# Kernel tuning notes

Measured on AMD Instinct MI355X. Metric: run time of the kernel, lower is better.

## Reference

```python
import jax, jax.numpy as jnp
import numpy as np

N_NODES = 100000
N_EDGES = 1600000
D = 32


def setup_inputs() -> dict:
    key = jax.random.key(0)
    k1, k2, k3, k4, k5, k6, k7 = jax.random.split(key, 7)
    x = jax.random.normal(k1, (N_NODES, D), dtype=jnp.float32)
    edge_index = jax.random.randint(k2, (2, N_EDGES), 0, N_NODES, dtype=jnp.int64)
    edge_weight = jax.random.uniform(k3, (N_EDGES,), dtype=jnp.float32)
    s = 1.0 / np.sqrt(D)
    W1 = jax.random.uniform(k4, (D, D), jnp.float32, -s, s)
    b1 = jax.random.uniform(k5, (D,), jnp.float32, -s, s)
    W2 = jax.random.uniform(k6, (D, D), jnp.float32, -s, s)
    b2 = jax.random.uniform(k7, (D,), jnp.float32, -s, s)
    return {"x": x, "edge_index": edge_index, "edge_weight": edge_weight,
            "W1": W1, "b1": b1, "W2": W2, "b2": b2}


def reference(x, edge_index, edge_weight, W1, b1, W2, b2):
    N = x.shape[0]
    src, dst = edge_index[0], edge_index[1]
    # gcn_norm with improved=True: self-loops get fill value 2.0
    loops = jnp.arange(N, dtype=edge_index.dtype)
    src_a = jnp.concatenate([src, loops])
    dst_a = jnp.concatenate([dst, loops])
    w_a = jnp.concatenate([edge_weight, jnp.full((N,), 2.0, x.dtype)])
    deg = jax.ops.segment_sum(w_a, dst_a, num_segments=N)          # [N]
    dinv = jnp.where(deg > 0, jax.lax.rsqrt(deg), 0.0)             # deg^-1/2, inf->0
    norm = dinv[src_a] * w_a * dinv[dst_a]                          # [E+N]

    def gcn_conv(h, W, b):
        h = h @ W                                                   # [N,D] dense transform
        msg = h[src_a] * norm[:, None]                              # gather + normalize [E+N,D]
        return jax.ops.segment_sum(msg, dst_a, num_segments=N) + b  # scatter-add + bias

    h = jax.nn.relu(gcn_conv(x, W1, b1))
    h = jax.nn.relu(gcn_conv(h, W2, b2))
    # F.dropout treated as identity (deterministic inference reference)
    return h
```

## Files before the change

kernel.cpp:

```cpp
#include <hip/hip_runtime.h>

#define D       32
#define BS      256
#define CBLK    500
#define CBLKP   500
#define BSH     7
#define BNODES  128
#define MAXBUCK 1024
#define SBUF_CAP 3584
#define ECAP    2560
#define POISON_BASE ((int)0xAAAAAAAAu)

__device__ inline unsigned bf16pack2(float a, float b) {
    unsigned ua = __float_as_uint(a);
    unsigned ub = __float_as_uint(b);
    ua = (ua + 0x7FFFu + ((ua >> 16) & 1)) >> 16;
    ub = (ub + 0x7FFFu + ((ub >> 16) & 1)) >> 16;
    return ua | (ub << 16);
}
__device__ inline uint2 bf16pack4(float4 v) {
    return make_uint2(bf16pack2(v.x, v.y), bf16pack2(v.z, v.w));
}
__device__ inline float4 bf16unpack4(uint2 h) {
    return make_float4(__uint_as_float(h.x << 16),
                       __uint_as_float(h.x & 0xFFFF0000u),
                       __uint_as_float(h.y << 16),
                       __uint_as_float(h.y & 0xFFFF0000u));
}

__device__ inline int lds_excl_scan(int* arr, int L, int* wsum, int t) {
    int carryv = 0;
    for (int base = 0; base < L; base += BS) {
        int idx = base + t;
        int v = (idx < L) ? arr[idx] : 0;
        int incl = v;
#pragma unroll
        for (int off = 1; off < 64; off <<= 1) {
            int u = __shfl_up(incl, off, 64);
            if ((t & 63) >= off) incl += u;
        }
        if ((t & 63) == 63) wsum[t >> 6] = incl;
        __syncthreads();
        int myw = t >> 6;
        int wpre = 0;
        if (myw > 0) wpre += wsum[0];
        if (myw > 1) wpre += wsum[1];
        if (myw > 2) wpre += wsum[2];
        int tot = wsum[0] + wsum[1] + wsum[2] + wsum[3];
        if (idx < L) arr[idx] = carryv + wpre + incl - v;
        __syncthreads();
        carryv += tot;
    }
    return carryv;
}

__global__ void k_localsort_gemm(const int* __restrict__ dst, const int* __restrict__ src,
                                 const float* __restrict__ w, int* __restrict__ bc,
                                 int* __restrict__ locoff, int2* __restrict__ staged,
                                 int E, int EPB, int NBUCK, int NBUCKP,
                                 const float* __restrict__ X, const float* __restrict__ Wm,
                                 uint2* __restrict__ H, int n) {
    __shared__ int    bins[MAXBUCK];
    __shared__ int    wsum[4];
    __shared__ int2   sbuf[SBUF_CAP];
    __shared__ float4 Ws[D * 8];
    int t = threadIdx.x;

    if ((int)blockIdx.x >= CBLK) {
        for (int i = t; i < D * 8; i += BS) Ws[i] = ((const float4*)Wm)[i];
        __syncthreads();
        int gid  = (blockIdx.x - CBLK) * BS + t;
        int node = gid >> 3;
        int q    = gid & 7;
        if (node >= n) return;
        float4 xv  = ((const float4*)X)[node * 8 + q];
        float4 acc = make_float4(0.f, 0.f, 0.f, 0.f);
#pragma unroll
        for (int k = 0; k < D; ++k) {
            float comp = (k & 3) == 0 ? xv.x : (k & 3) == 1 ? xv.y
                       : (k & 3) == 2 ? xv.z : xv.w;
            float  xk = __shfl(comp, k >> 2, 8);
            float4 wr = Ws[k * 8 + q];
            acc.x += xk * wr.x; acc.y += xk * wr.y;
            acc.z += xk * wr.z; acc.w += xk * wr.w;
        }
        H[node * 8 + q] = bf16pack4(acc);
        return;
    }

    int blk = blockIdx.x;
    int beg = blk * EPB;
    int end = min(E, beg + EPB);
    int cnt = end - beg;
    for (int i = t; i < NBUCK; i += BS) bins[i] = 0;
    __syncthreads();

    for (int e = beg + t; e < end; e += BS)
        atomicAdd(&bins[dst[e] >> BSH], 1);
    __syncthreads();
    for (int i = t; i < NBUCK; i += BS) bc[blk * NBUCKP + i] = bins[i];
    __syncthreads();
    lds_excl_scan(bins, NBUCK, wsum, t);
    for (int i = t; i < NBUCK; i += BS) locoff[blk * NBUCKP + i] = bins[i];
    __syncthreads();

    for (int e = beg + t; e < end; e += BS) {
        int dv  = dst[e];
        int b   = dv >> BSH;
        int pos = atomicAdd(&bins[b], 1);
        sbuf[pos] = make_int2(src[e] | ((dv & (BNODES - 1)) << 17), __float_as_int(w[e]));
    }
    __syncthreads();
    int2* myslice = staged + (size_t)blk * EPB;
    for (int i = t; i < cnt; i += BS) myslice[i] = sbuf[i];
}

__global__ void k_trans(const int* __restrict__ bc, const int* __restrict__ locoff,
                        int* __restrict__ bcT, int* __restrict__ locoffT,
                        int* __restrict__ btot, int NBUCK, int NBUCKP) {
    __shared__ int tile[32][33];
    const int* in  = (blockIdx.z == 0) ? bc  : locoff;
    int*       out = (blockIdx.z == 0) ? bcT : locoffT;
    int c0 = blockIdx.x * 32;
    int r0 = blockIdx.y * 32;
    int tx = threadIdx.x & 31, ty = threadIdx.x >> 5;
    for (int dy = ty; dy < 32; dy += 8) {
        int r = r0 + dy, c = c0 + tx;
        tile[dy][tx] = (r < CBLK && c < NBUCK) ? in[r * NBUCKP + c] : 0;
    }
    __syncthreads();
    for (int dy = ty; dy < 32; dy += 8) {
        int c = c0 + dy, r = r0 + tx;
        if (c < NBUCK && r < CBLK) out[c * CBLKP + r] = tile[tx][dy];
    }
    if (blockIdx.z == 0 && ty == 0 && c0 + tx < NBUCK) {
        int s = 0;
#pragma unroll
        for (int dy = 0; dy < 32; ++dy) s += tile[dy][tx];
        if (s) atomicAdd(&btot[c0 + tx], s);
    }
}

__global__ void k_merge(const int* __restrict__ bcT, const int* __restrict__ locoffT,
                        const int* __restrict__ btot, const int2* __restrict__ staged,
                        int2* __restrict__ emeta, int* __restrict__ rowptr,
                        float* __restrict__ dinv, uint2* __restrict__ H,
                        int N, int E, int NBUCK, int EPB) {
    __shared__ int2  ebuf[ECAP];
    __shared__ int   runoff[CBLK];
    __shared__ int   lrun[CBLK];
    __shared__ int   wsum[4];
    __shared__ int   ihist[BNODES];
    __shared__ float fdeg[BNODES];
    __shared__ int   cursor[BNODES];
    __shared__ float sdinv[BNODES];
    __shared__ int   hsum;
    int b = blockIdx.x, t = threadIdx.x;

    for (int k = t; k < CBLK; k += BS) {
        runoff[k] = bcT[b * CBLKP + k];
        lrun[k]   = locoffT[b * CBLKP + k];
    }
    if (t < BNODES) { ihist[t] = 0; fdeg[t] = 0.0f; }

    int pacc = 0;
    for (int k = t; k < b; k += BS) pacc += btot[k];
#pragma unroll
    for (int off = 32; off; off >>= 1) pacc += __shfl_down(pacc, off, 64);
    if ((t & 63) == 0) wsum[t >> 6] = pacc;
    __syncthreads();
    int bstart = wsum[0] + wsum[1] + wsum[2] + wsum[3];
    __syncthreads();

    int total = lds_excl_scan(runoff, CBLK, wsum, t);
    bool fits = total <= ECAP;

    if (fits) {
        int2 vnext = make_int2(0, 0);
        if (t < total) {
            int lo = 0, hi = CBLK - 1;
            while (lo < hi) {
                int mid = (lo + hi + 1) >> 1;
                if (runoff[mid] <= t) lo = mid; else hi = mid - 1;
            }
            vnext = staged[(size_t)lo * EPB + lrun[lo] + (t - runoff[lo])];
        }
        for (int p = t; p < total; p += BS) {
            int2 v = vnext;
            int pn = p + BS;
            if (pn < total) {
                int lo = 0, hi = CBLK - 1;
                while (lo < hi) {
                    int mid = (lo + hi + 1) >> 1;
                    if (runoff[mid] <= pn) lo = mid; else hi = mid - 1;
                }
                vnext = staged[(size_t)lo * EPB + lrun[lo] + (pn - runoff[lo])];
            }
            int local = (v.x >> 17) & (BNODES - 1);
            atomicAdd(&ihist[local], 1);
            atomicAdd(&fdeg[local], __int_as_float(v.y));
            ebuf[p] = v;
        }
    } else {
        for (int k = t; k < CBLK; k += BS) {
            int gs = runoff[k];
            int ge = (k + 1 < CBLK) ? runoff[k + 1] : total;
            const int2* run = staged + (size_t)k * EPB + lrun[k];
            for (int j = 0; j < ge - gs; ++j) {
                int2 v = run[j];
                int local = (v.x >> 17) & (BNODES - 1);
                atomicAdd(&ihist[local], 1);
                atomicAdd(&fdeg[local], __int_as_float(v.y));
            }
        }
    }
    __syncthreads();
    int v128 = 0, incl = 0;
    if (t < BNODES) {
        v128 = ihist[t];
        incl = v128;
#pragma unroll
        for (int off = 1; off < 64; off <<= 1) {
            int u = __shfl_up(incl, off, 64);
            if ((t & 63) >= off) incl += u;
        }
    }
    if (t == 63) hsum = incl;
    __syncthreads();
    if (t < BNODES) {
        if (t >= 64) incl += hsum;
        int excl = incl - v128;
        int node = b * BNODES + t;
        float di = rsqrtf(2.0f + fdeg[t]);
        if (node < N) {
            rowptr[node] = bstart + excl;
            dinv[node]   = di;
        }
        sdinv[t]  = di;
        cursor[t] = excl;
    }
    if (b == NBUCK - 1 && t == 0) rowptr[N] = E;
    __syncthreads();
    {
        int base_node = b * BNODES;
        for (int i = t; i < BNODES * 8; i += BS) {
            int row  = i >> 3;
            int node = base_node + row;
            if (node < N) {
                float di = sdinv[row];
                size_t off = (size_t)node * 8 + (i & 7);
                float4 f = bf16unpack4(H[off]);
                f.x *= di; f.y *= di; f.z *= di; f.w *= di;
                H[off] = bf16pack4(f);
            }
        }
    }
    __syncthreads();
    if (fits) {
        for (int p = t; p < total; p += BS) {
            int2 v = ebuf[p];
            int local = (v.x >> 17) & (BNODES - 1);
            int r = atomicAdd(&cursor[local], 1);
            emeta[bstart + r] = make_int2(v.x & 0x1FFFF, v.y);
        }
    } else {
        for (int k = t; k < CBLK; k += BS) {
            int gs = runoff[k];
            int ge = (k + 1 < CBLK) ? runoff[k + 1] : total;
            const int2* run = staged + (size_t)k * EPB + lrun[k];
            for (int j = 0; j < ge - gs; ++j) {
                int2 v = run[j];
                int local = (v.x >> 17) & (BNODES - 1);
                int r = atomicAdd(&cursor[local], 1);
                emeta[bstart + r] = make_int2(v.x & 0x1FFFF, v.y);
            }
        }
    }
}

template <bool FUSE_GEMM>
__global__ void k_agg(const int* __restrict__ rowptr, const int2* __restrict__ emeta,
                      const uint4* __restrict__ Hs, const float* __restrict__ dinv,
                      const float* __restrict__ b, const float* __restrict__ W2,
                      void* __restrict__ outv, int n) {
    __shared__ float4 Ws[D * 8];
    int tid = threadIdx.x;
    if (FUSE_GEMM) {
        for (int i = tid; i < D * 8; i += BS) Ws[i] = ((const float4*)W2)[i];
        __syncthreads();
    }

    int gid  = blockIdx.x * BS + tid;
    int node = gid >> 2;
    int q    = gid & 3;
    if (node >= n) return;

    float  di  = dinv[node];
    float4 bq0 = ((const float4*)b)[q * 2];
    float4 bq1 = ((const float4*)b)[q * 2 + 1];
    uint4  h0  = Hs[node * 4 + q];
    float4 a0  = bf16unpack4(make_uint2(h0.x, h0.y));
    float4 a1  = bf16unpack4(make_uint2(h0.z, h0.w));
    float4 acc0 = make_float4(2.f * a0.x, 2.f * a0.y, 2.f * a0.z, 2.f * a0.w);
    float4 acc1 = make_float4(2.f * a1.x, 2.f * a1.y, 2.f * a1.z, 2.f * a1.w);

    int beg  = rowptr[node];
    int end  = rowptr[node + 1];
    int full = beg + ((end - beg) & ~7);

    int2 em0, em1;
    if (beg < full) { em0 = emeta[beg + q]; em1 = emeta[beg + 4 + q]; }
    for (int i0 = beg; i0 < full; i0 += 8) {
        int2 cem0 = em0, cem1 = em1;
        if (i0 + 8 < full) { em0 = emeta[i0 + 8 + q]; em1 = emeta[i0 + 12 + q]; }
        float nm0 = __int_as_float(cem0.y);
        float nm1 = __int_as_float(cem1.y);
#pragma unroll
        for (int j = 0; j < 4; ++j) {
            int   s  = __shfl(cem0.x, j, 4);
            float nm = __shfl(nm0, j, 4);
            uint4 hv = Hs[s * 4 + q];
            float4 f0 = bf16unpack4(make_uint2(hv.x, hv.y));
            float4 f1 = bf16unpack4(make_uint2(hv.z, hv.w));
            acc0.x += nm * f0.x; acc0.y += nm * f0.y; acc0.z += nm * f0.z; acc0.w += nm * f0.w;
            acc1.x += nm * f1.x; acc1.y += nm * f1.y; acc1.z += nm * f1.z; acc1.w += nm * f1.w;
        }
#pragma unroll
        for (int j = 0; j < 4; ++j) {
            int   s  = __shfl(cem1.x, j, 4);
            float nm = __shfl(nm1, j, 4);
            uint4 hv = Hs[s * 4 + q];
            float4 f0 = bf16unpack4(make_uint2(hv.x, hv.y));
            float4 f1 = bf16unpack4(make_uint2(hv.z, hv.w));
            acc0.x += nm * f0.x; acc0.y += nm * f0.y; acc0.z += nm * f0.z; acc0.w += nm * f0.w;
            acc1.x += nm * f1.x; acc1.y += nm * f1.y; acc1.z += nm * f1.z; acc1.w += nm * f1.w;
        }
    }
    if (full < end) {
        int idx0 = full + q;
        int idx1 = full + 4 + q;
        int2 tm0 = (idx0 < end) ? emeta[idx0] : make_int2(0, 0);
        int2 tm1 = (idx1 < end) ? emeta[idx1] : make_int2(0, 0);
        float nm0 = (idx0 < end) ? __int_as_float(tm0.y) : 0.0f;
        float nm1 = (idx1 < end) ? __int_as_float(tm1.y) : 0.0f;
        int rem = end - full;
        int r0 = rem < 4 ? rem : 4;
        for (int j = 0; j < r0; ++j) {
            int   s  = __shfl(tm0.x, j, 4);
            float nm = __shfl(nm0, j, 4);
            uint4 hv = Hs[s * 4 + q];
            float4 f0 = bf16unpack4(make_uint2(hv.x, hv.y));
            float4 f1 = bf16unpack4(make_uint2(hv.z, hv.w));
            acc0.x += nm * f0.x; acc0.y += nm * f0.y; acc0.z += nm * f0.z; acc0.w += nm * f0.w;
            acc1.x += nm * f1.x; acc1.y += nm * f1.y; acc1.z += nm * f1.z; acc1.w += nm * f1.w;
        }
        for (int j = 0; j < rem - 4; ++j) {
            int   s  = __shfl(tm1.x, j, 4);
            float nm = __shfl(nm1, j, 4);
            uint4 hv = Hs[s * 4 + q];
            float4 f0 = bf16unpack4(make_uint2(hv.x, hv.y));
            float4 f1 = bf16unpack4(make_uint2(hv.z, hv.w));
            acc0.x += nm * f0.x; acc0.y += nm * f0.y; acc0.z += nm * f0.z; acc0.w += nm * f0.w;
            acc1.x += nm * f1.x; acc1.y += nm * f1.y; acc1.z += nm * f1.z; acc1.w += nm * f1.w;
        }
    }
    acc0.x = fmaxf(di * acc0.x + bq0.x, 0.f);
    acc0.y = fmaxf(di * acc0.y + bq0.y, 0.f);
    acc0.z = fmaxf(di * acc0.z + bq0.z, 0.f);
    acc0.w = fmaxf(di * acc0.w + bq0.w, 0.f);
    acc1.x = fmaxf(di * acc1.x + bq1.x, 0.f);
    acc1.y = fmaxf(di * acc1.y + bq1.y, 0.f);
    acc1.z = fmaxf(di * acc1.z + bq1.z, 0.f);
    acc1.w = fmaxf(di * acc1.w + bq1.w, 0.f);

    if (FUSE_GEMM) {
        float4 o0 = make_float4(0.f, 0.f, 0.f, 0.f);
        float4 o1 = make_float4(0.f, 0.f, 0.f, 0.f);
#pragma unroll
        for (int k = 0; k < D; ++k) {
            int sel = k & 7;
            float comp = sel == 0 ? acc0.x : sel == 1 ? acc0.y : sel == 2 ? acc0.z
                       : sel == 3 ? acc0.w : sel == 4 ? acc1.x : sel == 5 ? acc1.y
                       : sel == 6 ? acc1.z : acc1.w;
            float  hk = __shfl(comp, k >> 3, 4);
            float4 w0 = Ws[k * 8 + q * 2];
            float4 w1 = Ws[k * 8 + q * 2 + 1];
            o0.x += hk * w0.x; o0.y += hk * w0.y; o0.z += hk * w0.z; o0.w += hk * w0.w;
            o1.x += hk * w1.x; o1.y += hk * w1.y; o1.z += hk * w1.z; o1.w += hk * w1.w;
        }
        o0.x *= di; o0.y *= di; o0.z *= di; o0.w *= di;
        o1.x *= di; o1.y *= di; o1.z *= di; o1.w *= di;
        ((uint4*)outv)[node * 4 + q] =
            make_uint4(bf16pack2(o0.x, o0.y), bf16pack2(o0.z, o0.w),
                       bf16pack2(o1.x, o1.y), bf16pack2(o1.z, o1.w));
    } else {
        ((float4*)outv)[node * 8 + q * 2]     = acc0;
        ((float4*)outv)[node * 8 + q * 2 + 1] = acc1;
    }
}

__global__ void k_hist_gemm(const int4* __restrict__ dst4, int* __restrict__ cnt,
                            int4* __restrict__ rank4, int E4,
                            const float* __restrict__ X, const float* __restrict__ W,
                            uint2* __restrict__ H, int n, int gE4) {
    __shared__ float4 Ws[D * 8];
    int tid = threadIdx.x;
    if ((int)blockIdx.x < gE4) {
        int i = blockIdx.x * BS + tid;
        if (i >= E4) return;
        int4 d = dst4[i];
        int4 r;
        r.x = atomicAdd(&cnt[d.x], 1) - POISON_BASE;
        r.y = atomicAdd(&cnt[d.y], 1) - POISON_BASE;
        r.z = atomicAdd(&cnt[d.z], 1) - POISON_BASE;
        r.w = atomicAdd(&cnt[d.w], 1) - POISON_BASE;
        rank4[i] = r;
        return;
    }
    for (int i = tid; i < D * 8; i += BS) Ws[i] = ((const float4*)W)[i];
    __syncthreads();
    int gid  = (blockIdx.x - gE4) * BS + tid;
    int node = gid >> 3;
    int q    = gid & 7;
    if (node >= n) return;
    float4 xv  = ((const float4*)X)[node * 8 + q];
    float4 acc = make_float4(0.f, 0.f, 0.f, 0.f);
#pragma unroll
    for (int k = 0; k < D; ++k) {
        float comp = (k & 3) == 0 ? xv.x : (k & 3) == 1 ? xv.y
                   : (k & 3) == 2 ? xv.z : xv.w;
        float  xk = __shfl(comp, k >> 2, 8);
        float4 wr = Ws[k * 8 + q];
        acc.x += xk * wr.x; acc.y += xk * wr.y;
        acc.z += xk * wr.z; acc.w += xk * wr.w;
    }
    H[node * 8 + q] = bf16pack4(acc);
}

__global__ void k_scan1(const int* __restrict__ cnt, int* __restrict__ bsum, int n) {
    __shared__ int s[BS];
    int t = threadIdx.x, i = blockIdx.x * BS + t;
    s[t] = (i < n) ? (cnt[i] - POISON_BASE) : 0;
    __syncthreads();
    for (int off = BS / 2; off > 0; off >>= 1) {
        if (t < off) s[t] += s[t + off];
        __syncthreads();
    }
    if (t == 0) bsum[blockIdx.x] = s[0];
}

__global__ void k_scan23(const int* __restrict__ cnt, const int* __restrict__ bsum,
                         int* __restrict__ rowptr, int n) {
    __shared__ int red[BS];
    __shared__ int s[BS];
    int t = threadIdx.x, i = blockIdx.x * BS + t;
    int pacc = 0;
    for (int k = t; k < (int)blockIdx.x; k += BS) pacc += bsum[k];
    red[t] = pacc;
    __syncthreads();
    for (int off = BS / 2; off > 0; off >>= 1) {
        if (t < off) red[t] += red[t + off];
        __syncthreads();
    }
    int bpre = red[0];
    int v = (i < n) ? (cnt[i] - POISON_BASE) : 0;
    s[t] = v;
    __syncthreads();
    for (int off = 1; off < BS; off <<= 1) {
        int u = (t >= off) ? s[t - off] : 0;
        __syncthreads();
        s[t] += u;
        __syncthreads();
    }
    if (i < n) {
        int excl = bpre + s[t] - v;
        rowptr[i] = excl;
        if (i == n - 1) rowptr[n] = excl + v;
    }
}

__global__ void k_reorder(const int4* __restrict__ src4, const int4* __restrict__ dst4,
                          const float4* __restrict__ w4, const int4* __restrict__ rank4,
                          const int* __restrict__ rowptr, int2* __restrict__ emeta, int E4) {
    int i = blockIdx.x * blockDim.x + threadIdx.x;
    if (i >= E4) return;
    int4   s = src4[i];
    int4   d = dst4[i];
    float4 w = w4[i];
    int4   r = rank4[i];
    emeta[rowptr[d.x] + r.x] = make_int2(s.x, __float_as_int(w.x));
    emeta[rowptr[d.y] + r.y] = make_int2(s.y, __float_as_int(w.y));
    emeta[rowptr[d.z] + r.z] = make_int2(s.z, __float_as_int(w.z));
    emeta[rowptr[d.w] + r.w] = make_int2(s.w, __float_as_int(w.w));
}

__global__ void k_degscaleF(const int* __restrict__ rowptr, const int2* __restrict__ emeta,
                            float* __restrict__ dinv, uint2* __restrict__ H, int n) {
    int gid  = blockIdx.x * blockDim.x + threadIdx.x;
    int node = gid >> 3;
    int c    = gid & 7;
    if (node >= n) return;
    int beg = rowptr[node], end = rowptr[node + 1];
    float sum = 0.0f;
    for (int idx = beg + c; idx < end; idx += 8)
        sum += __int_as_float(emeta[idx].y);
    sum += __shfl_xor(sum, 4, 8);
    sum += __shfl_xor(sum, 2, 8);
    sum += __shfl_xor(sum, 1, 8);
    float di = rsqrtf(2.0f + sum);
    if (c == 0) dinv[node] = di;
    di = __shfl(di, 0, 8);
    size_t off = (size_t)node * 8 + c;
    float4 f = bf16unpack4(H[off]);
    f.x *= di; f.y *= di; f.z *= di; f.w *= di;
    H[off] = bf16pack4(f);
}

extern "C" void kernel_launch(void* const* d_in, const int* in_sizes, int n_in,
                              void* d_out, int out_size, void* d_ws, size_t ws_size,
                              hipStream_t stream) {
    const float* x   = (const float*)d_in[0];
    const int*   ei  = (const int*)d_in[1];
    const float* w   = (const float*)d_in[2];
    const float* W1  = (const float*)d_in[3];
    const float* b1  = (const float*)d_in[4];
    const float* W2  = (const float*)d_in[5];
    const float* b2  = (const float*)d_in[6];
    float*       out = (float*)d_out;

    const int N = in_sizes[0] / D;
    const int E = in_sizes[2];
    const int* src = ei;
    const int* dst = ei + E;

    const int NBUCK  = (N + BNODES - 1) / BNODES;
    const int NBUCKP = (NBUCK + 3) & ~3;
    const int EPB    = (E + CBLK - 1) / CBLK;
    const int NB     = (N + BS - 1) / BS;
    const int E4     = E / 4;
    const int gE4    = (E4 + BS - 1) / BS;
    const int gN8    = (N * 8 + BS - 1) / BS;
    const int gN4    = (N * 4 + BS - 1) / BS;

    char*  base    = (char*)d_ws;
    int2*  emeta   = (int2*)base;
    uint2* ht      = (uint2*)(base + (size_t)E * 8);
    uint2* ht2     = ht + (size_t)N * 8;
    float* dinv    = (float*)(ht2 + (size_t)N * 8);
    int*   rowptr  = (int*)(dinv + N);
    int2*  staged  = (int2*)(rowptr + ((N + 4) & ~3));
    int*   bc      = (int*)(staged + E);
    int*   locoff  = bc + (size_t)CBLK * NBUCKP;
    int*   bcT     = locoff + (size_t)CBLK * NBUCKP;
    int*   locoffT = bcT + (size_t)NBUCK * CBLKP;
    int*   btot    = locoffT + (size_t)NBUCK * CBLKP;
    size_t need    = (size_t)((char*)(btot + NBUCKP) - base);

    bool main_ok = (ws_size >= need) && (NBUCK <= MAXBUCK) && (N < (1 << 17)) &&
                   (EPB <= SBUF_CAP) && (N % 4 == 0);

    if (main_ok) {
        hipMemsetAsync(btot, 0, (size_t)NBUCKP * 4, stream);
        k_localsort_gemm<<<CBLK + gN8, BS, 0, stream>>>(dst, src, w, bc, locoff, staged,
                                                        E, EPB, NBUCK, NBUCKP, x, W1, ht, N);
        dim3 tg((NBUCK + 31) / 32, (CBLK + 31) / 32, 2);
        k_trans<<<tg, BS, 0, stream>>>(bc, locoff, bcT, locoffT, btot, NBUCK, NBUCKP);
        k_merge<<<NBUCK, BS, 0, stream>>>(bcT, locoffT, btot, staged, emeta, rowptr, dinv,
                                          ht, N, E, NBUCK, EPB);
        k_agg<true ><<<gN4, BS, 0, stream>>>(rowptr, emeta, (const uint4*)ht,  dinv, b1, W2, ht2, N);
        k_agg<false><<<gN4, BS, 0, stream>>>(rowptr, emeta, (const uint4*)ht2, dinv, b2, nullptr, out, N);
    } else {
        int* cnt  = (int*)staged;
        int* rank = cnt + N;
        int* bsum = rank + E;
        k_hist_gemm<<<gE4 + gN8, BS, 0, stream>>>((const int4*)dst, cnt, (int4*)rank, E4,
                                                  x, W1, ht, N, gE4);
        k_scan1 <<<NB, BS, 0, stream>>>(cnt, bsum, N);
        k_scan23<<<NB, BS, 0, stream>>>(cnt, bsum, rowptr, N);
        k_reorder<<<(E4 + BS - 1) / BS, BS, 0, stream>>>((const int4*)src, (const int4*)dst,
                                                         (const float4*)w, (const int4*)rank,
                                                         rowptr, emeta, E4);
        k_degscaleF<<<gN8, BS, 0, stream>>>(rowptr, emeta, dinv, ht, N);
        k_agg<true ><<<gN4, BS, 0, stream>>>(rowptr, emeta, (const uint4*)ht,  dinv, b1, W2, ht2, N);
        k_agg<false><<<gN4, BS, 0, stream>>>(rowptr, emeta, (const uint4*)ht2, dinv, b2, nullptr, out, N);
    }
}
```

Measured before the change: 186.2 us.

## Software-pipeline neighbor gathers in aggregation and cache dst in registers during local sort

The aggregation kernel now double-buffers 8-edge chunks: it issues all eight feature gathers for the next chunk before accumulating the current one, so more loads are in flight per thread. A launch-bounds hint is added to cap register use. The local sort keeps dst values in a register array so the scatter pass does not reload them, and a new guard checks that edges per block fit that array. The cost is much higher register pressure (16 uint4 gather buffers), which could reduce occupancy or cause spills.

```diff
diff --git a/kernel.cpp b/kernel.cpp
--- a/kernel.cpp
+++ b/kernel.cpp
@@ -8,6 +8,7 @@
 #define BNODES  128
 #define MAXBUCK 1024
 #define SBUF_CAP 3584
+#define MAX_EPT 13
 #define ECAP    2560
 #define POISON_BASE ((int)0xAAAAAAAAu)
 
@@ -95,8 +96,16 @@
     for (int i = t; i < NBUCK; i += BS) bins[i] = 0;
     __syncthreads();
 
-    for (int e = beg + t; e < end; e += BS)
-        atomicAdd(&bins[dst[e] >> BSH], 1);
+    int sdv[MAX_EPT];
+#pragma unroll
+    for (int i = 0; i < MAX_EPT; ++i) {
+        int e = beg + i * BS + t;
+        if (e < end) {
+            int dv = dst[e];
+            sdv[i] = dv;
+            atomicAdd(&bins[dv >> BSH], 1);
+        }
+    }
     __syncthreads();
     for (int i = t; i < NBUCK; i += BS) bc[blk * NBUCKP + i] = bins[i];
     __syncthreads();
@@ -104,11 +113,15 @@
     for (int i = t; i < NBUCK; i += BS) locoff[blk * NBUCKP + i] = bins[i];
     __syncthreads();
 
-    for (int e = beg + t; e < end; e += BS) {
-        int dv  = dst[e];
-        int b   = dv >> BSH;
-        int pos = atomicAdd(&bins[b], 1);
-        sbuf[pos] = make_int2(src[e] | ((dv & (BNODES - 1)) << 17), __float_as_int(w[e]));
+#pragma unroll
+    for (int i = 0; i < MAX_EPT; ++i) {
+        int e = beg + i * BS + t;
+        if (e < end) {
+            int dv  = sdv[i];
+            int b   = dv >> BSH;
+            int pos = atomicAdd(&bins[b], 1);
+            sbuf[pos] = make_int2(src[e] | ((dv & (BNODES - 1)) << 17), __float_as_int(w[e]));
+        }
     }
     __syncthreads();
     int2* myslice = staged + (size_t)blk * EPB;
@@ -278,11 +291,43 @@
     }
 }
 
+#define GATHER8(G0,G1,G2,G3,G4,G5,G6,G7,E0,E1)                         \
+    {                                                                  \
+        G0 = Hs[__shfl((E0).x, 0, 4) * 4 + q];                         \
+        G1 = Hs[__shfl((E0).x, 1, 4) * 4 + q];                         \
+        G2 = Hs[__shfl((E0).x, 2, 4) * 4 + q];                         \
+        G3 = Hs[__shfl((E0).x, 3, 4) * 4 + q];                         \
+        G4 = Hs[__shfl((E1).x, 0, 4) * 4 + q];                         \
+        G5 = Hs[__shfl((E1).x, 1, 4) * 4 + q];                         \
+        G6 = Hs[__shfl((E1).x, 2, 4) * 4 + q];                         \
+        G7 = Hs[__shfl((E1).x, 3, 4) * 4 + q];                         \
+    }
+#define FMA8(G, NM)                                                    \
+    {                                                                  \
+        float nm_ = (NM);                                              \
+        float4 f0_ = bf16unpack4(make_uint2((G).x, (G).y));            \
+        float4 f1_ = bf16unpack4(make_uint2((G).z, (G).w));            \
+        acc0.x += nm_ * f0_.x; acc0.y += nm_ * f0_.y;                  \
+        acc0.z += nm_ * f0_.z; acc0.w += nm_ * f0_.w;                  \
+        acc1.x += nm_ * f1_.x; acc1.y += nm_ * f1_.y;                  \
+        acc1.z += nm_ * f1_.z; acc1.w += nm_ * f1_.w;                  \
+    }
+#define ACCUM8(E0,E1,G0,G1,G2,G3,G4,G5,G6,G7)                          \
+    {                                                                  \
+        float nm0_ = __int_as_float((E0).y);                           \
+        float nm1_ = __int_as_float((E1).y);                           \
+        FMA8(G0, __shfl(nm0_, 0, 4)); FMA8(G1, __shfl(nm0_, 1, 4));    \
+        FMA8(G2, __shfl(nm0_, 2, 4)); FMA8(G3, __shfl(nm0_, 3, 4));    \
+        FMA8(G4, __shfl(nm1_, 0, 4)); FMA8(G5, __shfl(nm1_, 1, 4));    \
+        FMA8(G6, __shfl(nm1_, 2, 4)); FMA8(G7, __shfl(nm1_, 3, 4));    \
+    }
+
 template <bool FUSE_GEMM>
-__global__ void k_agg(const int* __restrict__ rowptr, const int2* __restrict__ emeta,
-                      const uint4* __restrict__ Hs, const float* __restrict__ dinv,
-                      const float* __restrict__ b, const float* __restrict__ W2,
-                      void* __restrict__ outv, int n) {
+__global__ __launch_bounds__(BS, 4)
+void k_agg(const int* __restrict__ rowptr, const int2* __restrict__ emeta,
+           const uint4* __restrict__ Hs, const float* __restrict__ dinv,
+           const float* __restrict__ b, const float* __restrict__ W2,
+           void* __restrict__ outv, int n) {
     __shared__ float4 Ws[D * 8];
     int tid = threadIdx.x;
     if (FUSE_GEMM) {
@@ -295,46 +340,43 @@
     int q    = gid & 3;
     if (node >= n) return;
 
-    float  di  = dinv[node];
-    float4 bq0 = ((const float4*)b)[q * 2];
-    float4 bq1 = ((const float4*)b)[q * 2 + 1];
-    uint4  h0  = Hs[node * 4 + q];
-    float4 a0  = bf16unpack4(make_uint2(h0.x, h0.y));
-    float4 a1  = bf16unpack4(make_uint2(h0.z, h0.w));
+    float  di = dinv[node];
+    uint4  h0 = Hs[node * 4 + q];
+    float4 a0 = bf16unpack4(make_uint2(h0.x, h0.y));
+    float4 a1 = bf16unpack4(make_uint2(h0.z, h0.w));
     float4 acc0 = make_float4(2.f * a0.x, 2.f * a0.y, 2.f * a0.z, 2.f * a0.w);
     float4 acc1 = make_float4(2.f * a1.x, 2.f * a1.y, 2.f * a1.z, 2.f * a1.w);
 
     int beg  = rowptr[node];
     int end  = rowptr[node + 1];
-    int full = beg + ((end - beg) & ~7);
-
-    int2 em0, em1;
-    if (beg < full) { em0 = emeta[beg + q]; em1 = emeta[beg + 4 + q]; }
-    for (int i0 = beg; i0 < full; i0 += 8) {
-        int2 cem0 = em0, cem1 = em1;
-        if (i0 + 8 < full) { em0 = emeta[i0 + 8 + q]; em1 = emeta[i0 + 12 + q]; }
-        float nm0 = __int_as_float(cem0.y);
-        float nm1 = __int_as_float(cem1.y);
-#pragma unroll
-        for (int j = 0; j < 4; ++j) {
-            int   s  = __shfl(cem0.x, j, 4);
-            float nm = __shfl(nm0, j, 4);
-            uint4 hv = Hs[s * 4 + q];
-            float4 f0 = bf16unpack4(make_uint2(hv.x, hv.y));
-            float4 f1 = bf16unpack4(make_uint2(hv.z, hv.w));
-            acc0.x += nm * f0.x; acc0.y += nm * f0.y; acc0.z += nm * f0.z; acc0.w += nm * f0.w;
-            acc1.x += nm * f1.x; acc1.y += nm * f1.y; acc1.z += nm * f1.z; acc1.w += nm * f1.w;
-        }
-#pragma unroll
-        for (int j = 0; j < 4; ++j) {
-            int   s  = __shfl(cem1.x, j, 4);
-            float nm = __shfl(nm1, j, 4);
-            uint4 hv = Hs[s * 4 + q];
-            float4 f0 = bf16unpack4(make_uint2(hv.x, hv.y));
-            float4 f1 = bf16unpack4(make_uint2(hv.z, hv.w));
-            acc0.x += nm * f0.x; acc0.y += nm * f0.y; acc0.z += nm * f0.z; acc0.w += nm * f0.w;
-            acc1.x += nm * f1.x; acc1.y += nm * f1.y; acc1.z += nm * f1.z; acc1.w += nm * f1.w;
-        }
+    int len  = end - beg;
+    int nch  = len >> 3;
+    int full = beg + (len & ~7);
+
+    uint4 ga0, ga1, ga2, ga3, ga4, ga5, ga6, ga7;
+    uint4 gb0, gb1, gb2, gb3, gb4, gb5, gb6, gb7;
+    int2 ea0, ea1, eb0 = make_int2(0, 0), eb1 = make_int2(0, 0);
+    int i0 = beg;
+    if (nch > 0) {
+        ea0 = emeta[i0 + q]; ea1 = emeta[i0 + 4 + q];
+        GATHER8(ga0, ga1, ga2, ga3, ga4, ga5, ga6, ga7, ea0, ea1);
+        if (nch > 1) { eb0 = emeta[i0 + 8 + q]; eb1 = emeta[i0 + 12 + q]; }
+    }
+    int c = 0;
+    for (; c + 2 <= nch; c += 2) {
+        GATHER8(gb0, gb1, gb2, gb3, gb4, gb5, gb6, gb7, eb0, eb1);
+        int2 ec0 = make_int2(0, 0), ec1 = ec0, ed0 = ec0, ed1 = ec0;
+        if (c + 2 < nch) { ec0 = emeta[i0 + 16 + q]; ec1 = emeta[i0 + 20 + q]; }
+        if (c + 3 < nch) { ed0 = emeta[i0 + 24 + q]; ed1 = emeta[i0 + 28 + q]; }
+        ACCUM8(ea0, ea1, ga0, ga1, ga2, ga3, ga4, ga5, ga6, ga7);
+        if (c + 2 < nch)
+            GATHER8(ga0, ga1, ga2, ga3, ga4, ga5, ga6, ga7, ec0, ec1);
+        ACCUM8(eb0, eb1, gb0, gb1, gb2, gb3, gb4, gb5, gb6, gb7);
+        ea0 = ec0; ea1 = ec1; eb0 = ed0; eb1 = ed1;
+        i0 += 16;
+    }
+    if (c < nch) {
+        ACCUM8(ea0, ea1, ga0, ga1, ga2, ga3, ga4, ga5, ga6, ga7);
     }
     if (full < end) {
         int idx0 = full + q;
@@ -349,21 +391,17 @@
             int   s  = __shfl(tm0.x, j, 4);
             float nm = __shfl(nm0, j, 4);
             uint4 hv = Hs[s * 4 + q];
-            float4 f0 = bf16unpack4(make_uint2(hv.x, hv.y));
-            float4 f1 = bf16unpack4(make_uint2(hv.z, hv.w));
-            acc0.x += nm * f0.x; acc0.y += nm * f0.y; acc0.z += nm * f0.z; acc0.w += nm * f0.w;
-            acc1.x += nm * f1.x; acc1.y += nm * f1.y; acc1.z += nm * f1.z; acc1.w += nm * f1.w;
+            FMA8(hv, nm);
         }
         for (int j = 0; j < rem - 4; ++j) {
             int   s  = __shfl(tm1.x, j, 4);
             float nm = __shfl(nm1, j, 4);
             uint4 hv = Hs[s * 4 + q];
-            float4 f0 = bf16unpack4(make_uint2(hv.x, hv.y));
-            float4 f1 = bf16unpack4(make_uint2(hv.z, hv.w));
-            acc0.x += nm * f0.x; acc0.y += nm * f0.y; acc0.z += nm * f0.z; acc0.w += nm * f0.w;
-            acc1.x += nm * f1.x; acc1.y += nm * f1.y; acc1.z += nm * f1.z; acc1.w += nm * f1.w;
-        }
-    }
+            FMA8(hv, nm);
+        }
+    }
+    float4 bq0 = ((const float4*)b)[q * 2];
+    float4 bq1 = ((const float4*)b)[q * 2 + 1];
     acc0.x = fmaxf(di * acc0.x + bq0.x, 0.f);
     acc0.y = fmaxf(di * acc0.y + bq0.y, 0.f);
     acc0.z = fmaxf(di * acc0.z + bq0.z, 0.f);
@@ -557,7 +595,7 @@
     size_t need    = (size_t)((char*)(btot + NBUCKP) - base);
 
     bool main_ok = (ws_size >= need) && (NBUCK <= MAXBUCK) && (N < (1 << 17)) &&
-                   (EPB <= SBUF_CAP) && (N % 4 == 0);
+                   (EPB <= SBUF_CAP) && ((EPB + BS - 1) / BS <= MAX_EPT) && (N % 4 == 0);
 
     if (main_ok) {
         hipMemsetAsync(btot, 0, (size_t)NBUCKP * 4, stream);
```

After: 213.7 us. 14.8% more time.
